# Kernel tuning notes

Hardware: AMD Instinct MI355X
Metric: run time of the kernel (lower is better)

The kernel has to match this reference:

```python
import jax, jax.numpy as jnp
import numpy as np

N = 2048
IN_DIM = 256
OUT_DIM = 64
N_HEADS = 8  # head_dim == n_heads required by a: Linear(2*n_heads, 1)
NEG_BIG = -9.0e15


def setup_inputs() -> dict:
    key = jax.random.key(0)
    k1, k2, k3, k4 = jax.random.split(key, 4)
    h = jax.random.normal(k1, (N, IN_DIM), dtype=jnp.float32)
    adj = jax.random.randint(k2, (N, N), 0, 2, dtype=jnp.int32)
    # xavier_uniform with gain=1.414 for W: bound = gain*sqrt(6/(fan_in+fan_out))
    bw = 1.414 * np.sqrt(6.0 / (IN_DIM + OUT_DIM))
    W_w = jax.random.uniform(k3, (OUT_DIM, IN_DIM), minval=-bw, maxval=bw, dtype=jnp.float32)
    W_b = jnp.zeros((OUT_DIM,), dtype=jnp.float32)
    ba = 1.414 * np.sqrt(6.0 / (2 * N_HEADS + 1))
    a_w = jax.random.uniform(k4, (1, 2 * N_HEADS), minval=-ba, maxval=ba, dtype=jnp.float32)
    a_b = jnp.zeros((1,), dtype=jnp.float32)
    return {"h": h, "adj": adj, "W_w": W_w, "W_b": W_b, "a_w": a_w, "a_b": a_b}


def reference(h, adj, W_w, W_b, a_w, a_b):
    H = a_w.shape[1] // 2
    out_dim = W_w.shape[0]
    Dh = out_dim // H  # == H by construction
    n = h.shape[0]
    wh = h @ W_w.T + W_b                      # [N, out_dim]
    wh_head = wh.reshape(n, H, Dh)            # [N, H, Dh]
    aL = a_w[0, :Dh]                           # applies to source node i features
    aR = a_w[0, Dh:]                           # applies to node j features
    e_i = jnp.einsum('nhd,d->nh', wh_head, aL)  # [N, H]
    e_j = jnp.einsum('nhd,d->nh', wh_head, aR)  # [N, H]
    # scores[i,j,h] without materializing the N*N concat tensor
    scores = e_i[:, None, :] + e_j[None, :, :] + a_b[0]   # [N, N, H]
    scores = jnp.where(scores >= 0, scores, 0.2 * scores)  # leaky_relu(0.2)
    masked = jnp.where(adj[:, :, None] > 0, scores, NEG_BIG)
    att = jax.nn.softmax(masked, axis=1)       # normalize over j
    # out[h,i,d] = sum_j att[i,j,h] * wh_head[j,h,d]
    out = jnp.einsum('ijh,jhd->hid', att, wh_head)  # [H, N, Dh]
    out = jax.nn.elu(out)
    return out.reshape(-1, out_dim)            # faithful to .view(-1, out_dim)
```

## Files before the change

kernel.cpp:

```cpp
#include <hip/hip_runtime.h>
#include <math.h>

#define NN 2048
#define INDIM 256
#define ODIM 64
#define NH 8
#define DHD 8
#define LOG2E 1.44269504088896340736f

__global__ __launch_bounds__(256) void gat_pre(
    const float* __restrict__ h, const float* __restrict__ Ww,
    const float* __restrict__ Wb, const float* __restrict__ aw,
    const float* __restrict__ ab,
    float* __restrict__ wh, float* __restrict__ eiL, float* __restrict__ ejL)
{
    __shared__ float sH[16][INDIM];
    const int t = threadIdx.x;
    const int n0 = blockIdx.x * 16;
    {
        const float4* src = (const float4*)(h + (size_t)n0 * INDIM);
        float4* dst = (float4*)&sH[0][0];
#pragma unroll
        for (int k = 0; k < 4; ++k) dst[t + k * 256] = src[t + k * 256];
    }
    __syncthreads();

    const int o  = t & 63;
    const int wv = t >> 6;
    const int nb = wv * 4;
    const float4* w4 = (const float4*)(Ww + (size_t)o * INDIM);
    float a0 = 0.f, a1 = 0.f, a2 = 0.f, a3 = 0.f;
#pragma unroll 4
    for (int k = 0; k < INDIM / 4; ++k) {
        const float4 wk = w4[k];
        const float4 h0 = *(const float4*)&sH[nb + 0][k * 4];
        const float4 h1 = *(const float4*)&sH[nb + 1][k * 4];
        const float4 h2 = *(const float4*)&sH[nb + 2][k * 4];
        const float4 h3 = *(const float4*)&sH[nb + 3][k * 4];
        a0 = fmaf(wk.x, h0.x, a0); a0 = fmaf(wk.y, h0.y, a0);
        a0 = fmaf(wk.z, h0.z, a0); a0 = fmaf(wk.w, h0.w, a0);
        a1 = fmaf(wk.x, h1.x, a1); a1 = fmaf(wk.y, h1.y, a1);
        a1 = fmaf(wk.z, h1.z, a1); a1 = fmaf(wk.w, h1.w, a1);
        a2 = fmaf(wk.x, h2.x, a2); a2 = fmaf(wk.y, h2.y, a2);
        a2 = fmaf(wk.z, h2.z, a2); a2 = fmaf(wk.w, h2.w, a2);
        a3 = fmaf(wk.x, h3.x, a3); a3 = fmaf(wk.y, h3.y, a3);
        a3 = fmaf(wk.z, h3.z, a3); a3 = fmaf(wk.w, h3.w, a3);
    }
    const float bias = Wb[o];
    float accs[4] = {a0 + bias, a1 + bias, a2 + bias, a3 + bias};

    const int d = o & 7;
    const float aL = aw[d], aR = aw[NH + d];
    const float abv = ab[0];
#pragma unroll
    for (int r = 0; r < 4; ++r) {
        const int n = n0 + nb + r;
        wh[(size_t)n * ODIM + o] = accs[r];
        float pi = accs[r] * aL;
        float pj = accs[r] * aR;
        pi += __shfl_xor(pi, 1, 64); pj += __shfl_xor(pj, 1, 64);
        pi += __shfl_xor(pi, 2, 64); pj += __shfl_xor(pj, 2, 64);
        pi += __shfl_xor(pi, 4, 64); pj += __shfl_xor(pj, 4, 64);
        if (d == 0) {
            const int hd = o >> 3;
            eiL[n * NH + hd] = (pi + abv) * LOG2E;
            ejL[n * NH + hd] = pj * LOG2E;
        }
    }
}

__global__ __launch_bounds__(512, 2) void gat_main(
    const int* __restrict__ adj, const float* __restrict__ wh,
    const float* __restrict__ eiL, const float* __restrict__ ejL,
    float* __restrict__ out)
{
    __shared__ float s_adj[8 * NN];
    __shared__ float s_red[8][8][8][9];
    const int t  = threadIdx.x;
    const int i0 = blockIdx.x * 8;

    {
        const int4* arow = (const int4*)(adj + (size_t)i0 * NN);
        float4* sa = (float4*)s_adj;
#pragma unroll
        for (int k = 0; k < 8; ++k) {
            const int4 v = arow[t + k * 512];
            sa[t + k * 512] = make_float4((float)v.x, (float)v.y, (float)v.z, (float)v.w);
        }
    }
    __syncthreads();

    const int hh = t & 7;
    const int jj = t >> 3;
    float eih[8];
#pragma unroll
    for (int i = 0; i < 8; ++i) eih[i] = eiL[(i0 + i) * NH + hh];

    float den[8];
    float acc[8][8];
#pragma unroll
    for (int i = 0; i < 8; ++i) {
        den[i] = 0.f;
#pragma unroll
        for (int d2 = 0; d2 < 8; ++d2) acc[i][d2] = 0.f;
    }

#pragma unroll 2
    for (int it = 0; it < NN / 64; ++it) {
        const int j = (it << 6) | jj;
        const float ejv = ejL[j * NH + hh];
        const float4* wr = (const float4*)(wh + (size_t)j * ODIM + hh * DHD);
        const float4 w0 = wr[0];
        const float4 w1 = wr[1];
#pragma unroll
        for (int i = 0; i < 8; ++i) {
            float s = eih[i] + ejv;
            s = fmaxf(s, 0.2f * s);
            float w = exp2f(s) * s_adj[i * NN + j];
            den[i] += w;
            acc[i][0] = fmaf(w, w0.x, acc[i][0]);
            acc[i][1] = fmaf(w, w0.y, acc[i][1]);
            acc[i][2] = fmaf(w, w0.z, acc[i][2]);
            acc[i][3] = fmaf(w, w0.w, acc[i][3]);
            acc[i][4] = fmaf(w, w1.x, acc[i][4]);
            acc[i][5] = fmaf(w, w1.y, acc[i][5]);
            acc[i][6] = fmaf(w, w1.z, acc[i][6]);
            acc[i][7] = fmaf(w, w1.w, acc[i][7]);
        }
    }

#pragma unroll
    for (int m = 8; m <= 32; m <<= 1) {
#pragma unroll
        for (int i = 0; i < 8; ++i) {
            den[i] += __shfl_xor(den[i], m, 64);
#pragma unroll
            for (int d2 = 0; d2 < 8; ++d2)
                acc[i][d2] += __shfl_xor(acc[i][d2], m, 64);
        }
    }
    const int lane = t & 63;
    const int wv   = t >> 6;
    if (lane < 8) {
#pragma unroll
        for (int i = 0; i < 8; ++i) {
#pragma unroll
            for (int d2 = 0; d2 < 8; ++d2) s_red[wv][lane][i][d2] = acc[i][d2];
            s_red[wv][lane][i][8] = den[i];
        }
    }
    __syncthreads();

    {
        const int i  = t >> 6;
        const int oh = (t >> 3) & 7;
        const int d2 = t & 7;
        float v = 0.f, dn = 0.f;
#pragma unroll
        for (int w2 = 0; w2 < 8; ++w2) {
            v  += s_red[w2][oh][i][d2];
            dn += s_red[w2][oh][i][8];
        }
        float r = v / dn;
        r = (r > 0.f) ? r : expm1f(r);
        out[(size_t)oh * (NN * DHD) + (size_t)(i0 + i) * DHD + d2] = r;
    }
}

extern "C" void kernel_launch(void* const* d_in, const int* in_sizes, int n_in,
                              void* d_out, int out_size, void* d_ws, size_t ws_size,
                              hipStream_t stream) {
    const float* h   = (const float*)d_in[0];
    const int*   adj = (const int*)d_in[1];
    const float* Ww  = (const float*)d_in[2];
    const float* Wb  = (const float*)d_in[3];
    const float* aw  = (const float*)d_in[4];
    const float* ab  = (const float*)d_in[5];
    float* out = (float*)d_out;

    float* wh  = (float*)d_ws;
    float* eiL = wh + (size_t)NN * ODIM;
    float* ejL = eiL + (size_t)NN * NH;

    gat_pre<<<NN / 16, 256, 0, stream>>>(h, Ww, Wb, aw, ab, wh, eiL, ejL);
    gat_main<<<NN / 8, 512, 0, stream>>>(adj, wh, eiL, ejL, out);
}
```

Baseline: 40.60 us.

## Bit-pack adjacency in shared memory and widen main kernel to 1024 threads

The main kernel now packs the 8 adjacency rows into one byte per column in shared memory instead of storing 8 float rows (64KB), and uses a bit test to mask the weights. Block size doubles to 1024 threads, with each thread covering half as many j iterations and the cross-wave reduction extended to 16 waves. The pre-kernel is split into twice as many blocks, each handling 8 rows, so it launches more parallel work. The aim is less LDS use, more parallelism per row group and more occupancy, at the cost of heavy register pressure under launch_bounds(1024,4) with 72 accumulators per thread, which may cause spills.

```diff
diff --git a/kernel.cpp b/kernel.cpp
--- a/kernel.cpp
+++ b/kernel.cpp
@@ -14,46 +14,40 @@
     const float* __restrict__ ab,
     float* __restrict__ wh, float* __restrict__ eiL, float* __restrict__ ejL)
 {
-    __shared__ float sH[16][INDIM];
+    __shared__ float sH[8][INDIM];
     const int t = threadIdx.x;
-    const int n0 = blockIdx.x * 16;
+    const int n0 = blockIdx.x * 8;
     {
         const float4* src = (const float4*)(h + (size_t)n0 * INDIM);
         float4* dst = (float4*)&sH[0][0];
-#pragma unroll
-        for (int k = 0; k < 4; ++k) dst[t + k * 256] = src[t + k * 256];
+        dst[t] = src[t];
+        dst[t + 256] = src[t + 256];
     }
     __syncthreads();
 
     const int o  = t & 63;
     const int wv = t >> 6;
-    const int nb = wv * 4;
+    const int nb = wv * 2;
     const float4* w4 = (const float4*)(Ww + (size_t)o * INDIM);
-    float a0 = 0.f, a1 = 0.f, a2 = 0.f, a3 = 0.f;
-#pragma unroll 4
+    float a0 = 0.f, a1 = 0.f;
+#pragma unroll 8
     for (int k = 0; k < INDIM / 4; ++k) {
         const float4 wk = w4[k];
         const float4 h0 = *(const float4*)&sH[nb + 0][k * 4];
         const float4 h1 = *(const float4*)&sH[nb + 1][k * 4];
-        const float4 h2 = *(const float4*)&sH[nb + 2][k * 4];
-        const float4 h3 = *(const float4*)&sH[nb + 3][k * 4];
         a0 = fmaf(wk.x, h0.x, a0); a0 = fmaf(wk.y, h0.y, a0);
         a0 = fmaf(wk.z, h0.z, a0); a0 = fmaf(wk.w, h0.w, a0);
         a1 = fmaf(wk.x, h1.x, a1); a1 = fmaf(wk.y, h1.y, a1);
         a1 = fmaf(wk.z, h1.z, a1); a1 = fmaf(wk.w, h1.w, a1);
-        a2 = fmaf(wk.x, h2.x, a2); a2 = fmaf(wk.y, h2.y, a2);
-        a2 = fmaf(wk.z, h2.z, a2); a2 = fmaf(wk.w, h2.w, a2);
-        a3 = fmaf(wk.x, h3.x, a3); a3 = fmaf(wk.y, h3.y, a3);
-        a3 = fmaf(wk.z, h3.z, a3); a3 = fmaf(wk.w, h3.w, a3);
     }
     const float bias = Wb[o];
-    float accs[4] = {a0 + bias, a1 + bias, a2 + bias, a3 + bias};
+    float accs[2] = {a0 + bias, a1 + bias};
 
     const int d = o & 7;
     const float aL = aw[d], aR = aw[NH + d];
     const float abv = ab[0];
 #pragma unroll
-    for (int r = 0; r < 4; ++r) {
+    for (int r = 0; r < 2; ++r) {
         const int n = n0 + nb + r;
         wh[(size_t)n * ODIM + o] = accs[r];
         float pi = accs[r] * aL;
@@ -69,24 +63,26 @@
     }
 }
 
-__global__ __launch_bounds__(512, 2) void gat_main(
+__global__ __launch_bounds__(1024, 4) void gat_main(
     const int* __restrict__ adj, const float* __restrict__ wh,
     const float* __restrict__ eiL, const float* __restrict__ ejL,
     float* __restrict__ out)
 {
-    __shared__ float s_adj[8 * NN];
-    __shared__ float s_red[8][8][8][9];
+    __shared__ unsigned char s_bits[NN];
+    __shared__ float s_red[16][8][8][9];
     const int t  = threadIdx.x;
     const int i0 = blockIdx.x * 8;
 
     {
-        const int4* arow = (const int4*)(adj + (size_t)i0 * NN);
-        float4* sa = (float4*)s_adj;
+        unsigned int b0 = 0, b1 = 0;
 #pragma unroll
-        for (int k = 0; k < 8; ++k) {
-            const int4 v = arow[t + k * 512];
-            sa[t + k * 512] = make_float4((float)v.x, (float)v.y, (float)v.z, (float)v.w);
+        for (int i = 0; i < 8; ++i) {
+            const int2 v = *(const int2*)(adj + (size_t)(i0 + i) * NN + 2 * t);
+            b0 |= (v.x != 0) << i;
+            b1 |= (v.y != 0) << i;
         }
+        s_bits[2 * t]     = (unsigned char)b0;
+        s_bits[2 * t + 1] = (unsigned char)b1;
     }
     __syncthreads();
 
@@ -105,9 +101,9 @@
         for (int d2 = 0; d2 < 8; ++d2) acc[i][d2] = 0.f;
     }
 
-#pragma unroll 2
-    for (int it = 0; it < NN / 64; ++it) {
-        const int j = (it << 6) | jj;
+    for (int it = 0; it < NN / 128; ++it) {
+        const int j = (it << 7) | jj;
+        const int bits = s_bits[j];
         const float ejv = ejL[j * NH + hh];
         const float4* wr = (const float4*)(wh + (size_t)j * ODIM + hh * DHD);
         const float4 w0 = wr[0];
@@ -116,7 +112,8 @@
         for (int i = 0; i < 8; ++i) {
             float s = eih[i] + ejv;
             s = fmaxf(s, 0.2f * s);
-            float w = exp2f(s) * s_adj[i * NN + j];
+            const float e = exp2f(s);
+            const float w = (bits & (1 << i)) ? e : 0.0f;
             den[i] += w;
             acc[i][0] = fmaf(w, w0.x, acc[i][0]);
             acc[i][1] = fmaf(w, w0.y, acc[i][1]);
@@ -151,13 +148,13 @@
     }
     __syncthreads();
 
-    {
+    if (t < 512) {
         const int i  = t >> 6;
         const int oh = (t >> 3) & 7;
         const int d2 = t & 7;
         float v = 0.f, dn = 0.f;
 #pragma unroll
-        for (int w2 = 0; w2 < 8; ++w2) {
+        for (int w2 = 0; w2 < 16; ++w2) {
             v  += s_red[w2][oh][i][d2];
             dn += s_red[w2][oh][i][8];
         }
@@ -182,6 +179,6 @@
     float* eiL = wh + (size_t)NN * ODIM;
     float* ejL = eiL + (size_t)NN * NH;
 
-    gat_pre<<<NN / 16, 256, 0, stream>>>(h, Ww, Wb, aw, ab, wh, eiL, ejL);
-    gat_main<<<NN / 8, 512, 0, stream>>>(adj, wh, eiL, ejL, out);
+    gat_pre<<<NN / 8, 256, 0, stream>>>(h, Ww, Wb, aw, ab, wh, eiL, ejL);
+    gat_main<<<NN / 8, 1024, 0, stream>>>(adj, wh, eiL, ejL, out);
 }
```

After: 46.53 us. 14.6% more time.
